# Kernel tuning notes

Measured on AMD Instinct MI355X. Metric: run time of the kernel, lower is better.

Reference implementation:

```python
import jax, jax.numpy as jnp
import numpy as np

B, SQ, SK, TT, DM, H, HKV, D, FF = 1, 2048, 3072, 4096, 2048, 16, 8, 128, 6144
EPS = 1e-6
THETA = 1000000.0

def rmsnorm(x, w):
    v = jnp.mean(x * x, axis=-1, keepdims=True)
    return x * jax.lax.rsqrt(v + EPS) * w

def rope_cos_sin(pos):
    inv = 1.0 / (THETA ** (jnp.arange(0, D, 2, dtype=jnp.float32) / D))
    f = pos.astype(jnp.float32)[..., None] * inv  # [B,S,D/2]
    emb = jnp.concatenate([f, f], axis=-1)        # [B,S,D]
    return jnp.cos(emb), jnp.sin(emb)

def rotate_half(x):
    x1, x2 = jnp.split(x, 2, axis=-1)
    return jnp.concatenate([-x2, x1], axis=-1)

def apply_rope(x, cos, sin):  # x: [B,H,S,D]; cos/sin: [B,S,D]
    return x * cos[:, None] + rotate_half(x) * sin[:, None]

def setup_inputs() -> dict:
    ks = jax.random.split(jax.random.key(0), 16)
    p = lambda i, sh: jax.random.normal(ks[i], sh, jnp.float32) * 0.02
    sri = lambda i, sh, mx: jnp.sort(jax.random.randint(ks[i], sh, 0, mx))
    return dict(
        hidden_states=jax.random.normal(ks[0], (B, SQ, DM), jnp.float32),
        kv_hidden=jax.random.normal(ks[1], (B, SK, DM), jnp.float32),
        causal_mask=jax.random.normal(ks[2], (B, 1, TT, TT), jnp.float32),
        w_q=p(3, (DM, H * D)), w_k=p(4, (DM, HKV * D)), w_v=p(5, (DM, HKV * D)),
        w_o=p(6, (H * D, DM)),
        q_norm_w=jnp.ones((D,), jnp.float32), k_norm_w=jnp.ones((D,), jnp.float32),
        ln1_w=jnp.ones((DM,), jnp.float32), ln2_w=jnp.ones((DM,), jnp.float32),
        w_gate=p(7, (DM, FF)), w_up=p(8, (DM, FF)), w_down=p(9, (FF, DM)),
        positions=sri(10, (B, SQ), TT), kv_positions=sri(11, (B, SK), TT),
        hs_idxs=sri(12, (SQ,), TT), key_idxs=sri(13, (SK,), TT))

def reference(hidden_states, kv_hidden, causal_mask, w_q, w_k, w_v, w_o,
              q_norm_w, k_norm_w, ln1_w, ln2_w, w_gate, w_up, w_down,
              positions, kv_positions, hs_idxs, key_idxs):
    # irregular mask reconstruction: gather kv dim then query dim (dims 3 then 2)
    mask = causal_mask[:, :, :, key_idxs][:, :, hs_idxs, :]  # [B,1,SQ,SK]
    # input_layernorm (RMSNorm)
    h = rmsnorm(hidden_states, ln1_w)
    hk = rmsnorm(kv_hidden, ln1_w)
    # Qwen3 attention: proj + per-head RMSNorm on q/k + RoPE + GQA
    q = rmsnorm((h @ w_q).reshape(B, SQ, H, D), q_norm_w).transpose(0, 2, 1, 3)
    k = rmsnorm((hk @ w_k).reshape(B, SK, HKV, D), k_norm_w).transpose(0, 2, 1, 3)
    v = (hk @ w_v).reshape(B, SK, HKV, D).transpose(0, 2, 1, 3)
    cq, sq = rope_cos_sin(positions)
    ck, sk = rope_cos_sin(kv_positions)
    q = apply_rope(q, cq, sq)
    k = apply_rope(k, ck, sk)
    rep = H // HKV
    k = jnp.repeat(k, rep, axis=1)
    v = jnp.repeat(v, rep, axis=1)
    scores = jnp.einsum('bhqd,bhkd->bhqk', q, k) * (D ** -0.5) + mask
    attn = jax.nn.softmax(scores, axis=-1)
    ctx = jnp.einsum('bhqk,bhkd->bhqd', attn, v).transpose(0, 2, 1, 3).reshape(B, SQ, H * D)
    hidden = hidden_states + ctx @ w_o
    # post-attention RMSNorm + SwiGLU MLP
    h2 = rmsnorm(hidden, ln2_w)
    mlp = (jax.nn.silu(h2 @ w_gate) * (h2 @ w_up)) @ w_down
    return hidden + mlp
```

## Files before the change

### kernel.cpp

```cpp
#include <hip/hip_runtime.h>
#include <math.h>

constexpr int SQ = 2048, SK = 3072, TT = 4096, DM = 2048;
constexpr int H = 16, HKV = 8, D = 128, FF = 6144;
#define EPS 1e-6f

typedef __attribute__((ext_vector_type(8))) short short8;
typedef __attribute__((ext_vector_type(4))) float f32x4;

#define GLOBAL_AS __attribute__((address_space(1)))
#define LDS_AS __attribute__((address_space(3)))

__device__ __forceinline__ unsigned short f2bf(float f) {
  unsigned u = __float_as_uint(f);
  unsigned r = (u + 0x7fffu + ((u >> 16) & 1u)) >> 16;
  return (unsigned short)r;
}
__device__ __forceinline__ float bflo(unsigned w) { return __uint_as_float(w << 16); }
__device__ __forceinline__ float bfhi(unsigned w) { return __uint_as_float(w & 0xffff0000u); }

__global__ __launch_bounds__(256) void wt_bf16_kernel(
    const float* __restrict__ w, unsigned short* __restrict__ wT, int K, int N) {
  __shared__ unsigned short s[64][73];
  int n0 = blockIdx.x * 64, k0 = blockIdx.y * 64;
  int tid = threadIdx.x;
  int cn = (tid & 15) * 4, rk = tid >> 4;
#pragma unroll
  for (int p = 0; p < 4; p++) {
    int k = rk + p * 16;
    const float4 f = *(const float4*)&w[(size_t)(k0 + k) * N + n0 + cn];
    s[k][cn] = f2bf(f.x); s[k][cn + 1] = f2bf(f.y);
    s[k][cn + 2] = f2bf(f.z); s[k][cn + 3] = f2bf(f.w);
  }
  __syncthreads();
  int ck = (tid & 15) * 4, rn = tid >> 4;
#pragma unroll
  for (int p = 0; p < 4; p++) {
    int n = rn + p * 16;
    ushort4 o;
    o.x = s[ck][n]; o.y = s[ck + 1][n]; o.z = s[ck + 2][n]; o.w = s[ck + 3][n];
    *(ushort4*)&wT[(size_t)(n0 + n) * K + k0 + ck] = o;
  }
}

__global__ __launch_bounds__(256) void vtrans_kernel(
    const float* __restrict__ vb, unsigned short* __restrict__ vt) {
  __shared__ unsigned short s[64][72];
  int kv0 = blockIdx.x * 64, d0 = blockIdx.y * 64, kvh = blockIdx.z;
  int tid = threadIdx.x;
  int cd = (tid & 15) * 4, rk = tid >> 4;
#pragma unroll
  for (int p = 0; p < 4; p++) {
    int kv = rk + p * 16;
    const float4 f = *(const float4*)&vb[((size_t)(kv0 + kv) * HKV + kvh) * D + d0 + cd];
    s[kv][cd] = f2bf(f.x); s[kv][cd + 1] = f2bf(f.y);
    s[kv][cd + 2] = f2bf(f.z); s[kv][cd + 3] = f2bf(f.w);
  }
  __syncthreads();
  int ck = (tid & 15) * 4, rd = tid >> 4;
#pragma unroll
  for (int p = 0; p < 4; p++) {
    int d = rd + p * 16;
    ushort4 o;
    o.x = s[ck][d]; o.y = s[ck + 1][d]; o.z = s[ck + 2][d]; o.w = s[ck + 3][d];
    *(ushort4*)&vt[((size_t)kvh * D + d0 + d) * SK + kv0 + ck] = o;
  }
}

__global__ __launch_bounds__(256) void rmsnorm_bf16_kernel(
    const float* __restrict__ x, const float* __restrict__ w,
    unsigned short* __restrict__ y) {
  int row = blockIdx.x;
  const float* xr = x + (size_t)row * DM;
  int c = threadIdx.x * 8;
  float4 a = *(const float4*)&xr[c];
  float4 b = *(const float4*)&xr[c + 4];
  float ss = a.x * a.x + a.y * a.y + a.z * a.z + a.w * a.w +
             b.x * b.x + b.y * b.y + b.z * b.z + b.w * b.w;
  for (int o = 32; o > 0; o >>= 1) ss += __shfl_down(ss, o);
  __shared__ float sred[4];
  int lane = threadIdx.x & 63, wid = threadIdx.x >> 6;
  if (lane == 0) sred[wid] = ss;
  __syncthreads();
  if (threadIdx.x == 0)
    sred[0] = rsqrtf((sred[0] + sred[1] + sred[2] + sred[3]) * (1.0f / (float)DM) + EPS);
  __syncthreads();
  float sc = sred[0];
  float4 wa = *(const float4*)&w[c];
  float4 wb = *(const float4*)&w[c + 4];
  ushort4 o1, o2;
  o1.x = f2bf(a.x * sc * wa.x); o1.y = f2bf(a.y * sc * wa.y);
  o1.z = f2bf(a.z * sc * wa.z); o1.w = f2bf(a.w * sc * wa.w);
  o2.x = f2bf(b.x * sc * wb.x); o2.y = f2bf(b.y * sc * wb.y);
  o2.z = f2bf(b.z * sc * wb.z); o2.w = f2bf(b.w * sc * wb.w);
  unsigned short* yr = y + (size_t)row * DM + c;
  *(ushort4*)&yr[0] = o1;
  *(ushort4*)&yr[4] = o2;
}

template <bool ADD, bool OUTBF>
__global__ __launch_bounds__(256) void mgemm_kernel(
    const unsigned short* __restrict__ A, const unsigned short* __restrict__ BT,
    const float* __restrict__ Add, void* __restrict__ Cp,
    int M, int N, int K) {
  __shared__ unsigned short As[128 * 64];
  __shared__ unsigned short Bs[128 * 64];
  const int tid = threadIdx.x;
  const int wave = tid >> 6, lane = tid & 63;
  const int bm = blockIdx.y * 128, bn = blockIdx.x * 128;
  const int wr = wave >> 1, wc = wave & 1;
  const int fl = lane & 15, fk = lane >> 4;

  const int srow = wave * 8 + (lane >> 3);
  const int schunk = (lane & 7) ^ (srow & 7);
  const unsigned short* Abase = A + (size_t)(bm + srow) * K + schunk * 8;
  const unsigned short* Bbase = BT + (size_t)(bn + srow) * K + schunk * 8;

  f32x4 acc[4][4];
#pragma unroll
  for (int m = 0; m < 4; m++)
#pragma unroll
    for (int n = 0; n < 4; n++)
#pragma unroll
      for (int e = 0; e < 4; e++) acc[m][n][e] = 0.f;

  for (int k0 = 0; k0 < K; k0 += 64) {
#pragma unroll
    for (int p = 0; p < 4; p++) {
      __builtin_amdgcn_global_load_lds(
          (GLOBAL_AS unsigned*)(Abase + (size_t)(p * 32) * K + k0),
          (LDS_AS unsigned*)&As[(p * 32 + wave * 8) * 64], 16, 0, 0);
      __builtin_amdgcn_global_load_lds(
          (GLOBAL_AS unsigned*)(Bbase + (size_t)(p * 32) * K + k0),
          (LDS_AS unsigned*)&Bs[(p * 32 + wave * 8) * 64], 16, 0, 0);
    }
    __syncthreads();
#pragma unroll
    for (int kk = 0; kk < 2; kk++) {
      short8 a_[4], b_[4];
#pragma unroll
      for (int m = 0; m < 4; m++) {
        int row = wr * 64 + m * 16 + fl;
        int ch = (kk * 4 + fk) ^ (row & 7);
        a_[m] = *(const short8*)&As[row * 64 + ch * 8];
      }
#pragma unroll
      for (int n = 0; n < 4; n++) {
        int row = wc * 64 + n * 16 + fl;
        int ch = (kk * 4 + fk) ^ (row & 7);
        b_[n] = *(const short8*)&Bs[row * 64 + ch * 8];
      }
#pragma unroll
      for (int m = 0; m < 4; m++)
#pragma unroll
        for (int n = 0; n < 4; n++)
          acc[m][n] = __builtin_amdgcn_mfma_f32_16x16x32_bf16(
              a_[m], b_[n], acc[m][n], 0, 0, 0);
    }
    __syncthreads();
  }

#pragma unroll
  for (int m = 0; m < 4; m++) {
    int row0 = bm + wr * 64 + m * 16 + fk * 4;
#pragma unroll
    for (int n = 0; n < 4; n++) {
      int col = bn + wc * 64 + n * 16 + fl;
#pragma unroll
      for (int r = 0; r < 4; r++) {
        size_t idx = (size_t)(row0 + r) * N + col;
        float v = acc[m][n][r];
        if (ADD) v += Add[idx];
        if (OUTBF) ((unsigned short*)Cp)[idx] = f2bf(v);
        else ((float*)Cp)[idx] = v;
      }
    }
  }
}

__global__ __launch_bounds__(128) void qknorm_rope_bf16_kernel(
    const float* __restrict__ x, const float* __restrict__ nw,
    const int* __restrict__ pos, unsigned short* __restrict__ out,
    int nheads, int S) {
  int s = blockIdx.x, hh = blockIdx.y;
  const float* xr = x + ((size_t)s * nheads + hh) * D;
  int d = threadIdx.x;
  float vv = xr[d];
  float ss = vv * vv;
  for (int o = 32; o > 0; o >>= 1) ss += __shfl_down(ss, o);
  __shared__ float sred[2];
  __shared__ float sn[D];
  if ((d & 63) == 0) sred[d >> 6] = ss;
  __syncthreads();
  float ms = (sred[0] + sred[1]) * (1.0f / (float)D);
  float n = vv * rsqrtf(ms + EPS) * nw[d];
  sn[d] = n;
  __syncthreads();
  int t = d & 63;
  float inv = powf(1000000.0f, -((float)(2 * t)) / (float)D);
  float ang = (float)pos[s] * inv;
  float c = cosf(ang), si = sinf(ang);
  float rh = (d < 64) ? -sn[d + 64] : sn[d - 64];
  out[((size_t)hh * S + s) * D + d] = f2bf(n * c + rh * si);
}

__global__ __launch_bounds__(256) void mask_gather_kernel(
    const float* __restrict__ mask, const int* __restrict__ hs_idxs,
    const int* __restrict__ key_idxs, float* __restrict__ maskg) {
  int q = blockIdx.x;
  const float* base = mask + (size_t)hs_idxs[q] * TT;
  float* out = maskg + (size_t)q * SK;
  for (int j = threadIdx.x; j < SK; j += 256) out[j] = base[key_idxs[j]];
}

__global__ __launch_bounds__(256) void attn_mfma_kernel(
    const unsigned short* __restrict__ qbf, const unsigned short* __restrict__ kbf,
    const unsigned short* __restrict__ vtbf, const float* __restrict__ maskg,
    unsigned short* __restrict__ ctx) {
  __shared__ unsigned short Ks[2][64 * 128];
  __shared__ unsigned short Vts[2][128 * 64];
  __shared__ unsigned short Pl[4][16 * 72];

  const int tid = threadIdx.x;
  const int wave = tid >> 6, lane = tid & 63;
  const int fl = lane & 15, g = lane >> 4;
  const float scale = 0.08838834764831845f;

  int bid = blockIdx.x;
  int swz = (bid & 7) * 64 + (bid >> 3);
  const int hh = swz >> 5;
  const int qblk = (swz & 31) * 64;
  const int kvh = hh >> 1;

  short8 qf[4];
  {
    const unsigned short* qrow = qbf + ((size_t)hh * SQ + qblk + wave * 16 + fl) * D;
#pragma unroll
    for (int kw = 0; kw < 4; kw++) qf[kw] = *(const short8*)&qrow[kw * 32 + g * 8];
  }

  const unsigned short* ksrc[4];
  const unsigned short* vsrc[4];
  {
    int krow = lane >> 4;
    int vrow = lane >> 3;
    int vcs = (lane & 7) ^ vrow;
#pragma unroll
    for (int p = 0; p < 4; p++) {
      int rowk = wave * 16 + p * 4 + krow;
      int kcs = (lane & 15) ^ (rowk & 7);
      ksrc[p] = kbf + ((size_t)kvh * SK + rowk) * D + kcs * 8;
      int rowv = wave * 32 + p * 8 + vrow;
      vsrc[p] = vtbf + ((size_t)kvh * D + rowv) * SK + vcs * 8;
    }
  }
  const float* mbase = maskg + (size_t)(qblk + wave * 16 + fl) * SK + g * 4;

  float m_i = -INFINITY, l_i = 0.f;
  f32x4 o[8];
#pragma unroll
  for (int n = 0; n < 8; n++)
#pragma unroll
    for (int r = 0; r < 4; r++) o[n][r] = 0.f;

#define STAGE(bufi)                                                            \
  {                                                                            \
    _Pragma("unroll")                                                          \
    for (int p = 0; p < 4; p++) {                                              \
      __builtin_amdgcn_global_load_lds(                                        \
          (GLOBAL_AS unsigned*)ksrc[p],                                        \
          (LDS_AS unsigned*)&Ks[bufi][(wave * 16 + p * 4) * 128], 16, 0, 0);   \
      __builtin_amdgcn_global_load_lds(                                        \
          (GLOBAL_AS unsigned*)vsrc[p],                                        \
          (LDS_AS unsigned*)&Vts[bufi][(wave * 32 + p * 8) * 64], 16, 0, 0);   \
      ksrc[p] += 64 * D;                                                       \
      vsrc[p] += 64;                                                           \
    }                                                                          \
  }

  STAGE(0);
  __syncthreads();

  const int NT = SK / 64;
  for (int t = 0; t < NT; t++) {
    const int buf = t & 1;
    if (t + 1 < NT) STAGE(buf ^ 1);

    float4 mv[4];
#pragma unroll
    for (int kvf = 0; kvf < 4; kvf++) mv[kvf] = *(const float4*)(mbase + kvf * 16);
    mbase += 64;

    f32x4 sa[4];
#pragma unroll
    for (int kvf = 0; kvf < 4; kvf++)
#pragma unroll
      for (int r = 0; r < 4; r++) sa[kvf][r] = 0.f;
#pragma unroll
    for (int kw = 0; kw < 4; kw++) {
#pragma unroll
      for (int kvf = 0; kvf < 4; kvf++) {
        int row = kvf * 16 + fl;
        int ch = (kw * 4 + g) ^ (fl & 7);
        short8 kf = *(const short8*)&Ks[buf][row * 128 + ch * 8];
        sa[kvf] = __builtin_amdgcn_mfma_f32_16x16x32_bf16(kf, qf[kw], sa[kvf], 0, 0, 0);
      }
    }

    float p4[4][4];
    float rm = -INFINITY;
#pragma unroll
    for (int kvf = 0; kvf < 4; kvf++) {
      p4[kvf][0] = sa[kvf][0] * scale + mv[kvf].x;
      p4[kvf][1] = sa[kvf][1] * scale + mv[kvf].y;
      p4[kvf][2] = sa[kvf][2] * scale + mv[kvf].z;
      p4[kvf][3] = sa[kvf][3] * scale + mv[kvf].w;
#pragma unroll
      for (int r = 0; r < 4; r++) rm = fmaxf(rm, p4[kvf][r]);
    }
    rm = fmaxf(rm, __shfl_xor(rm, 16));
    rm = fmaxf(rm, __shfl_xor(rm, 32));
    float mn = fmaxf(m_i, rm);
    float alpha = __expf(m_i - mn);
    m_i = mn;
    float rs = 0.f;
#pragma unroll
    for (int kvf = 0; kvf < 4; kvf++) {
#pragma unroll
      for (int r = 0; r < 4; r++) { p4[kvf][r] = __expf(p4[kvf][r] - mn); rs += p4[kvf][r]; }
      ushort4 pk;
      pk.x = f2bf(p4[kvf][0]); pk.y = f2bf(p4[kvf][1]);
      pk.z = f2bf(p4[kvf][2]); pk.w = f2bf(p4[kvf][3]);
      *(ushort4*)&Pl[wave][fl * 72 + kvf * 16 + g * 4] = pk;
    }
    rs += __shfl_xor(rs, 16);
    rs += __shfl_xor(rs, 32);
    l_i = l_i * alpha + rs;

    float av[4];
#pragma unroll
    for (int r = 0; r < 4; r++) av[r] = __shfl(alpha, 4 * g + r);
#pragma unroll
    for (int n = 0; n < 8; n++)
#pragma unroll
      for (int r = 0; r < 4; r++) o[n][r] *= av[r];

#pragma unroll
    for (int k = 0; k < 2; k++) {
      short8 pf = *(const short8*)&Pl[wave][fl * 72 + k * 32 + g * 8];
#pragma unroll
      for (int n = 0; n < 8; n++) {
        int row = n * 16 + fl;
        int ch = (k * 4 + g) ^ (fl & 7);
        short8 vf = *(const short8*)&Vts[buf][row * 64 + ch * 8];
        o[n] = __builtin_amdgcn_mfma_f32_16x16x32_bf16(pf, vf, o[n], 0, 0, 0);
      }
    }
    __syncthreads();
  }

#pragma unroll
  for (int r = 0; r < 4; r++) {
    float linv = 1.f / __shfl(l_i, 4 * g + r);
    size_t base = ((size_t)(qblk + wave * 16 + 4 * g + r)) * (H * D) + (size_t)hh * D + fl;
#pragma unroll
    for (int n = 0; n < 8; n++) ctx[base + n * 16] = f2bf(o[n][r] * linv);
  }
#undef STAGE
}

__device__ __forceinline__ unsigned silu2(unsigned gw, unsigned uw) {
  float g0 = bflo(gw), g1 = bfhi(gw), u0 = bflo(uw), u1 = bfhi(uw);
  float r0 = g0 / (1.f + __expf(-g0)) * u0;
  float r1 = g1 / (1.f + __expf(-g1)) * u1;
  return ((unsigned)f2bf(r1) << 16) | f2bf(r0);
}
__global__ __launch_bounds__(256) void silu_mul_bf16_kernel(
    unsigned short* __restrict__ g, const unsigned short* __restrict__ u, int n8) {
  int i = blockIdx.x * 256 + threadIdx.x;
  if (i >= n8) return;
  uint4 G = *(const uint4*)&g[(size_t)i * 8];
  uint4 U = *(const uint4*)&u[(size_t)i * 8];
  G.x = silu2(G.x, U.x); G.y = silu2(G.y, U.y);
  G.z = silu2(G.z, U.z); G.w = silu2(G.w, U.w);
  *(uint4*)&g[(size_t)i * 8] = G;
}

extern "C" void kernel_launch(void* const* d_in, const int* in_sizes, int n_in,
                              void* d_out, int out_size, void* d_ws, size_t ws_size,
                              hipStream_t stream) {
  (void)in_sizes; (void)n_in; (void)out_size; (void)ws_size;
  const float* hidden_states = (const float*)d_in[0];
  const float* kv_hidden     = (const float*)d_in[1];
  const float* causal_mask   = (const float*)d_in[2];
  const float* w_q      = (const float*)d_in[3];
  const float* w_k      = (const float*)d_in[4];
  const float* w_v      = (const float*)d_in[5];
  const float* w_o      = (const float*)d_in[6];
  const float* q_norm_w = (const float*)d_in[7];
  const float* k_norm_w = (const float*)d_in[8];
  const float* ln1_w    = (const float*)d_in[9];
  const float* ln2_w    = (const float*)d_in[10];
  const float* w_gate   = (const float*)d_in[11];
  const float* w_up     = (const float*)d_in[12];
  const float* w_down   = (const float*)d_in[13];
  const int* positions    = (const int*)d_in[14];
  const int* kv_positions = (const int*)d_in[15];
  const int* hs_idxs      = (const int*)d_in[16];
  const int* key_idxs     = (const int*)d_in[17];

  char* wsb = (char*)d_ws;
  float* maskg           = (float*)(wsb + 0);
  unsigned short* h_bf   = (unsigned short*)(wsb + 25165824);
  unsigned short* hk_bf  = (unsigned short*)(wsb + 33554432);
  unsigned short* W1     = (unsigned short*)(wsb + 46137344);
  unsigned short* W2     = (unsigned short*)(wsb + 71303168);
  float* qb              = (float*)(wsb + 96468992);
  float* kb              = (float*)(wsb + 113246208);
  float* vb              = (float*)(wsb + 125829120);
  unsigned short* ctx_bf = (unsigned short*)(wsb + 138412032);
  unsigned short* gate_bf = (unsigned short*)wsb;
  unsigned short* up_bf   = (unsigned short*)(wsb + 113246208);
  float* hidden           = qb;
  unsigned short* h2_bf   = h_bf;
  unsigned short* qbf    = (unsigned short*)(wsb + 46137344);
  unsigned short* kbf    = (unsigned short*)(wsb + 54525952);
  unsigned short* vtbf   = (unsigned short*)(wsb + 60817408);

  mask_gather_kernel<<<SQ, 256, 0, stream>>>(causal_mask, hs_idxs, key_idxs, maskg);
  rmsnorm_bf16_kernel<<<SQ, 256, 0, stream>>>(hidden_states, ln1_w, h_bf);
  rmsnorm_bf16_kernel<<<SK, 256, 0, stream>>>(kv_hidden, ln1_w, hk_bf);

  wt_bf16_kernel<<<dim3((H * D) / 64, DM / 64), 256, 0, stream>>>(w_q, W1, DM, H * D);
  wt_bf16_kernel<<<dim3((HKV * D) / 64, DM / 64), 256, 0, stream>>>(w_k, W2, DM, HKV * D);
  mgemm_kernel<false, false><<<dim3((H * D) / 128, SQ / 128), 256, 0, stream>>>(
      h_bf, W1, nullptr, qb, SQ, H * D, DM);
  mgemm_kernel<false, false><<<dim3((HKV * D) / 128, SK / 128), 256, 0, stream>>>(
      hk_bf, W2, nullptr, kb, SK, HKV * D, DM);
  wt_bf16_kernel<<<dim3((HKV * D) / 64, DM / 64), 256, 0, stream>>>(w_v, W1, DM, HKV * D);
  mgemm_kernel<false, false><<<dim3((HKV * D) / 128, SK / 128), 256, 0, stream>>>(
      hk_bf, W1, nullptr, vb, SK, HKV * D, DM);

  qknorm_rope_bf16_kernel<<<dim3(SQ, H), 128, 0, stream>>>(
      qb, q_norm_w, positions, qbf, H, SQ);
  qknorm_rope_bf16_kernel<<<dim3(SK, HKV), 128, 0, stream>>>(
      kb, k_norm_w, kv_positions, kbf, HKV, SK);
  vtrans_kernel<<<dim3(SK / 64, D / 64, HKV), 256, 0, stream>>>(vb, vtbf);

  attn_mfma_kernel<<<512, 256, 0, stream>>>(qbf, kbf, vtbf, maskg, ctx_bf);

  wt_bf16_kernel<<<dim3(DM / 64, (H * D) / 64), 256, 0, stream>>>(w_o, W2, H * D, DM);
  mgemm_kernel<true, false><<<dim3(DM / 128, SQ / 128), 256, 0, stream>>>(
      ctx_bf, W2, hidden_states, hidden, SQ, DM, H * D);

  rmsnorm_bf16_kernel<<<SQ, 256, 0, stream>>>(hidden, ln2_w, h2_bf);
  wt_bf16_kernel<<<dim3(FF / 64, DM / 64), 256, 0, stream>>>(w_gate, W1, DM, FF);
  wt_bf16_kernel<<<dim3(FF / 64, DM / 64), 256, 0, stream>>>(w_up, W2, DM, FF);
  mgemm_kernel<false, true><<<dim3(FF / 128, SQ / 128), 256, 0, stream>>>(
      h2_bf, W1, nullptr, gate_bf, SQ, FF, DM);
  mgemm_kernel<false, true><<<dim3(FF / 128, SQ / 128), 256, 0, stream>>>(
      h2_bf, W2, nullptr, up_bf, SQ, FF, DM);
  silu_mul_bf16_kernel<<<(SQ * FF / 8 + 255) / 256, 256, 0, stream>>>(
      gate_bf, up_bf, SQ * FF / 8);

  wt_bf16_kernel<<<dim3(DM / 64, FF / 64), 256, 0, stream>>>(w_down, W1, FF, DM);
  mgemm_kernel<true, false><<<dim3(DM / 128, SQ / 128), 256, 0, stream>>>(
      gate_bf, W1, hidden, (float*)d_out, SQ, DM, FF);
}
```

Measured before the change: 892.1 us.

## Split-K small GEMMs with atomics, fuse K/V and gate/up GEMMs, lazy softmax rescale

The Q, O and down projections now use a split-K GEMM that accumulates into pre-zeroed or pre-copied fp32 outputs with atomic adds. This fills more compute units, since these grids had only 256 tiles. K and V projections are merged into one GEMM over concatenated weights, and gate and up are computed in a single launch with a dual-output GEMM. The attention kernel skips the running-max rescale unless some row's max grows by more than 8, which avoids extra exps and multiplies at the cost of reduced numerical headroom. The atomics make accumulation order nondeterministic, and the new zero and copy passes add memory traffic.

```diff
diff --git a/kernel.cpp b/kernel.cpp
--- a/kernel.cpp
+++ b/kernel.cpp
@@ -44,7 +44,7 @@
 }
 
 __global__ __launch_bounds__(256) void vtrans_kernel(
-    const float* __restrict__ vb, unsigned short* __restrict__ vt) {
+    const float* __restrict__ vb, int ldv, unsigned short* __restrict__ vt) {
   __shared__ unsigned short s[64][72];
   int kv0 = blockIdx.x * 64, d0 = blockIdx.y * 64, kvh = blockIdx.z;
   int tid = threadIdx.x;
@@ -52,7 +52,7 @@
 #pragma unroll
   for (int p = 0; p < 4; p++) {
     int kv = rk + p * 16;
-    const float4 f = *(const float4*)&vb[((size_t)(kv0 + kv) * HKV + kvh) * D + d0 + cd];
+    const float4 f = *(const float4*)&vb[(size_t)(kv0 + kv) * ldv + kvh * D + d0 + cd];
     s[kv][cd] = f2bf(f.x); s[kv][cd + 1] = f2bf(f.y);
     s[kv][cd + 2] = f2bf(f.z); s[kv][cd + 3] = f2bf(f.w);
   }
@@ -98,23 +98,29 @@
   *(ushort4*)&yr[4] = o2;
 }
 
-template <bool ADD, bool OUTBF>
+template <bool OUTBF>
 __global__ __launch_bounds__(256) void mgemm_kernel(
-    const unsigned short* __restrict__ A, const unsigned short* __restrict__ BT,
-    const float* __restrict__ Add, void* __restrict__ Cp,
+    const unsigned short* __restrict__ A, const unsigned short* __restrict__ BT1,
+    const unsigned short* __restrict__ BT2, int N1,
+    void* __restrict__ C1p, void* __restrict__ C2p, int ld1, int ld2,
     int M, int N, int K) {
   __shared__ unsigned short As[128 * 64];
   __shared__ unsigned short Bs[128 * 64];
   const int tid = threadIdx.x;
   const int wave = tid >> 6, lane = tid & 63;
   const int bm = blockIdx.y * 128, bn = blockIdx.x * 128;
+  const bool second = bn >= N1;
+  const unsigned short* BT = second ? BT2 : BT1;
+  const int bnl = second ? bn - N1 : bn;
+  void* Cp = second ? C2p : C1p;
+  const int ldc = second ? ld2 : ld1;
   const int wr = wave >> 1, wc = wave & 1;
   const int fl = lane & 15, fk = lane >> 4;
 
   const int srow = wave * 8 + (lane >> 3);
   const int schunk = (lane & 7) ^ (srow & 7);
   const unsigned short* Abase = A + (size_t)(bm + srow) * K + schunk * 8;
-  const unsigned short* Bbase = BT + (size_t)(bn + srow) * K + schunk * 8;
+  const unsigned short* Bbase = BT + (size_t)(bnl + srow) * K + schunk * 8;
 
   f32x4 acc[4][4];
 #pragma unroll
@@ -165,12 +171,11 @@
     int row0 = bm + wr * 64 + m * 16 + fk * 4;
 #pragma unroll
     for (int n = 0; n < 4; n++) {
-      int col = bn + wc * 64 + n * 16 + fl;
+      int col = bnl + wc * 64 + n * 16 + fl;
 #pragma unroll
       for (int r = 0; r < 4; r++) {
-        size_t idx = (size_t)(row0 + r) * N + col;
+        size_t idx = (size_t)(row0 + r) * ldc + col;
         float v = acc[m][n][r];
-        if (ADD) v += Add[idx];
         if (OUTBF) ((unsigned short*)Cp)[idx] = f2bf(v);
         else ((float*)Cp)[idx] = v;
       }
@@ -178,12 +183,95 @@
   }
 }
 
+__global__ __launch_bounds__(256) void msplit_kernel(
+    const unsigned short* __restrict__ A, const unsigned short* __restrict__ BT,
+    float* __restrict__ C, int M, int N, int K, int kchunk) {
+  __shared__ unsigned short As[128 * 64];
+  __shared__ unsigned short Bs[128 * 64];
+  const int tid = threadIdx.x;
+  const int wave = tid >> 6, lane = tid & 63;
+  const int bm = blockIdx.y * 128, bn = blockIdx.x * 128;
+  const int kbeg = blockIdx.z * kchunk, kend = kbeg + kchunk;
+  const int wr = wave >> 1, wc = wave & 1;
+  const int fl = lane & 15, fk = lane >> 4;
+
+  const int srow = wave * 8 + (lane >> 3);
+  const int schunk = (lane & 7) ^ (srow & 7);
+  const unsigned short* Abase = A + (size_t)(bm + srow) * K + schunk * 8;
+  const unsigned short* Bbase = BT + (size_t)(bn + srow) * K + schunk * 8;
+
+  f32x4 acc[4][4];
+#pragma unroll
+  for (int m = 0; m < 4; m++)
+#pragma unroll
+    for (int n = 0; n < 4; n++)
+#pragma unroll
+      for (int e = 0; e < 4; e++) acc[m][n][e] = 0.f;
+
+  for (int k0 = kbeg; k0 < kend; k0 += 64) {
+#pragma unroll
+    for (int p = 0; p < 4; p++) {
+      __builtin_amdgcn_global_load_lds(
+          (GLOBAL_AS unsigned*)(Abase + (size_t)(p * 32) * K + k0),
+          (LDS_AS unsigned*)&As[(p * 32 + wave * 8) * 64], 16, 0, 0);
+      __builtin_amdgcn_global_load_lds(
+          (GLOBAL_AS unsigned*)(Bbase + (size_t)(p * 32) * K + k0),
+          (LDS_AS unsigned*)&Bs[(p * 32 + wave * 8) * 64], 16, 0, 0);
+    }
+    __syncthreads();
+#pragma unroll
+    for (int kk = 0; kk < 2; kk++) {
+      short8 a_[4], b_[4];
+#pragma unroll
+      for (int m = 0; m < 4; m++) {
+        int row = wr * 64 + m * 16 + fl;
+        int ch = (kk * 4 + fk) ^ (row & 7);
+        a_[m] = *(const short8*)&As[row * 64 + ch * 8];
+      }
+#pragma unroll
+      for (int n = 0; n < 4; n++) {
+        int row = wc * 64 + n * 16 + fl;
+        int ch = (kk * 4 + fk) ^ (row & 7);
+        b_[n] = *(const short8*)&Bs[row * 64 + ch * 8];
+      }
+#pragma unroll
+      for (int m = 0; m < 4; m++)
+#pragma unroll
+        for (int n = 0; n < 4; n++)
+          acc[m][n] = __builtin_amdgcn_mfma_f32_16x16x32_bf16(
+              a_[m], b_[n], acc[m][n], 0, 0, 0);
+    }
+    __syncthreads();
+  }
+
+#pragma unroll
+  for (int m = 0; m < 4; m++) {
+    int row0 = bm + wr * 64 + m * 16 + fk * 4;
+#pragma unroll
+    for (int n = 0; n < 4; n++) {
+      int col = bn + wc * 64 + n * 16 + fl;
+#pragma unroll
+      for (int r = 0; r < 4; r++)
+        unsafeAtomicAdd(&C[(size_t)(row0 + r) * N + col], acc[m][n][r]);
+    }
+  }
+}
+
+__global__ __launch_bounds__(256) void zero4_kernel(float4* __restrict__ p, int n4) {
+  int i = blockIdx.x * 256 + threadIdx.x;
+  if (i < n4) p[i] = make_float4(0.f, 0.f, 0.f, 0.f);
+}
+__global__ __launch_bounds__(256) void copy4_kernel(
+    float4* __restrict__ d, const float4* __restrict__ s, int n4) {
+  int i = blockIdx.x * 256 + threadIdx.x;
+  if (i < n4) d[i] = s[i];
+}
+
 __global__ __launch_bounds__(128) void qknorm_rope_bf16_kernel(
-    const float* __restrict__ x, const float* __restrict__ nw,
-    const int* __restrict__ pos, unsigned short* __restrict__ out,
-    int nheads, int S) {
+    const float* __restrict__ x, int ldx, const float* __restrict__ nw,
+    const int* __restrict__ pos, unsigned short* __restrict__ out, int S) {
   int s = blockIdx.x, hh = blockIdx.y;
-  const float* xr = x + ((size_t)s * nheads + hh) * D;
+  const float* xr = x + (size_t)s * ldx + hh * D;
   int d = threadIdx.x;
   float vv = xr[d];
   float ss = vv * vv;
@@ -320,8 +408,9 @@
     }
     rm = fmaxf(rm, __shfl_xor(rm, 16));
     rm = fmaxf(rm, __shfl_xor(rm, 32));
-    float mn = fmaxf(m_i, rm);
-    float alpha = __expf(m_i - mn);
+    const int need = __any(rm > m_i + 8.f);
+    float mn = need ? fmaxf(m_i, rm) : m_i;
+    float alpha = need ? __expf(m_i - mn) : 1.f;
     m_i = mn;
     float rs = 0.f;
 #pragma unroll
@@ -337,13 +426,15 @@
     rs += __shfl_xor(rs, 32);
     l_i = l_i * alpha + rs;
 
-    float av[4];
-#pragma unroll
-    for (int r = 0; r < 4; r++) av[r] = __shfl(alpha, 4 * g + r);
-#pragma unroll
-    for (int n = 0; n < 8; n++)
-#pragma unroll
-      for (int r = 0; r < 4; r++) o[n][r] *= av[r];
+    if (need) {
+      float av[4];
+#pragma unroll
+      for (int r = 0; r < 4; r++) av[r] = __shfl(alpha, 4 * g + r);
+#pragma unroll
+      for (int n = 0; n < 8; n++)
+#pragma unroll
+        for (int r = 0; r < 4; r++) o[n][r] *= av[r];
+    }
 
 #pragma unroll
     for (int k = 0; k < 2; k++) {
@@ -413,57 +504,64 @@
   float* maskg           = (float*)(wsb + 0);
   unsigned short* h_bf   = (unsigned short*)(wsb + 25165824);
   unsigned short* hk_bf  = (unsigned short*)(wsb + 33554432);
-  unsigned short* W1     = (unsigned short*)(wsb + 46137344);
-  unsigned short* W2     = (unsigned short*)(wsb + 71303168);
-  float* qb              = (float*)(wsb + 96468992);
-  float* kb              = (float*)(wsb + 113246208);
-  float* vb              = (float*)(wsb + 125829120);
-  unsigned short* ctx_bf = (unsigned short*)(wsb + 138412032);
-  unsigned short* gate_bf = (unsigned short*)wsb;
-  unsigned short* up_bf   = (unsigned short*)(wsb + 113246208);
-  float* hidden           = qb;
-  unsigned short* h2_bf   = h_bf;
-  unsigned short* qbf    = (unsigned short*)(wsb + 46137344);
-  unsigned short* kbf    = (unsigned short*)(wsb + 54525952);
-  unsigned short* vtbf   = (unsigned short*)(wsb + 60817408);
+  unsigned short* Wq     = (unsigned short*)(wsb + 46137344);
+  unsigned short* Wkv    = (unsigned short*)(wsb + 54525952);
+  float* qb              = (float*)(wsb + 62914560);
+  float* kvb             = (float*)(wsb + 79691776);
+  unsigned short* qbf    = (unsigned short*)(wsb + 104857600);
+  unsigned short* kbf    = (unsigned short*)(wsb + 113246208);
+  unsigned short* vtbf   = (unsigned short*)(wsb + 119537664);
+  unsigned short* ctx_bf = (unsigned short*)(wsb + 125829120);
+  float* hidden          = qb;
+  unsigned short* Wo     = Wq;
+  unsigned short* h2_bf  = h_bf;
+  unsigned short* Wg     = (unsigned short*)(wsb + 0);
+  unsigned short* Wu     = (unsigned short*)(wsb + 79691776);
+  unsigned short* gate_bf = (unsigned short*)(wsb + 104857600);
+  unsigned short* up_bf  = (unsigned short*)(wsb + 33554432);
+  unsigned short* Wd     = (unsigned short*)(wsb + 33554432);
 
   mask_gather_kernel<<<SQ, 256, 0, stream>>>(causal_mask, hs_idxs, key_idxs, maskg);
   rmsnorm_bf16_kernel<<<SQ, 256, 0, stream>>>(hidden_states, ln1_w, h_bf);
   rmsnorm_bf16_kernel<<<SK, 256, 0, stream>>>(kv_hidden, ln1_w, hk_bf);
 
-  wt_bf16_kernel<<<dim3((H * D) / 64, DM / 64), 256, 0, stream>>>(w_q, W1, DM, H * D);
-  wt_bf16_kernel<<<dim3((HKV * D) / 64, DM / 64), 256, 0, stream>>>(w_k, W2, DM, HKV * D);
-  mgemm_kernel<false, false><<<dim3((H * D) / 128, SQ / 128), 256, 0, stream>>>(
-      h_bf, W1, nullptr, qb, SQ, H * D, DM);
-  mgemm_kernel<false, false><<<dim3((HKV * D) / 128, SK / 128), 256, 0, stream>>>(
-      hk_bf, W2, nullptr, kb, SK, HKV * D, DM);
-  wt_bf16_kernel<<<dim3((HKV * D) / 64, DM / 64), 256, 0, stream>>>(w_v, W1, DM, HKV * D);
-  mgemm_kernel<false, false><<<dim3((HKV * D) / 128, SK / 128), 256, 0, stream>>>(
-      hk_bf, W1, nullptr, vb, SK, HKV * D, DM);
+  wt_bf16_kernel<<<dim3((H * D) / 64, DM / 64), 256, 0, stream>>>(w_q, Wq, DM, H * D);
+  wt_bf16_kernel<<<dim3((HKV * D) / 64, DM / 64), 256, 0, stream>>>(w_k, Wkv, DM, HKV * D);
+  wt_bf16_kernel<<<dim3((HKV * D) / 64, DM / 64), 256, 0, stream>>>(
+      w_v, Wkv + (size_t)(HKV * D) * DM, DM, HKV * D);
+
+  zero4_kernel<<<(SQ * H * D / 4 + 255) / 256, 256, 0, stream>>>((float4*)qb, SQ * H * D / 4);
+  msplit_kernel<<<dim3((H * D) / 128, SQ / 128, 2), 256, 0, stream>>>(
+      h_bf, Wq, qb, SQ, H * D, DM, DM / 2);
+  mgemm_kernel<false><<<dim3((2 * HKV * D) / 128, SK / 128), 256, 0, stream>>>(
+      hk_bf, Wkv, nullptr, 2 * HKV * D, kvb, nullptr, 2 * HKV * D, 0, SK, 2 * HKV * D, DM);
 
   qknorm_rope_bf16_kernel<<<dim3(SQ, H), 128, 0, stream>>>(
-      qb, q_norm_w, positions, qbf, H, SQ);
+      qb, H * D, q_norm_w, positions, qbf, SQ);
   qknorm_rope_bf16_kernel<<<dim3(SK, HKV), 128, 0, stream>>>(
-      kb, k_norm_w, kv_positions, kbf, HKV, SK);
-  vtrans_kernel<<<dim3(SK / 64, D / 64, HKV), 256, 0, stream>>>(vb, vtbf);
+      kvb, 2 * HKV * D, k_norm_w, kv_positions, kbf, SK);
+  vtrans_kernel<<<dim3(SK / 64, D / 64, HKV), 256, 0, stream>>>(
+      kvb + HKV * D, 2 * HKV * D, vtbf);
 
   attn_mfma_kernel<<<512, 256, 0, stream>>>(qbf, kbf, vtbf, maskg, ctx_bf);
 
-  wt_bf16_kernel<<<dim3(DM / 64, (H * D) / 64), 256, 0, stream>>>(w_o, W2, H * D, DM);
-  mgemm_kernel<true, false><<<dim3(DM / 128, SQ / 128), 256, 0, stream>>>(
-      ctx_bf, W2, hidden_states, hidden, SQ, DM, H * D);
+  copy4_kernel<<<(SQ * DM / 4 + 255) / 256, 256, 0, stream>>>(
+      (float4*)hidden, (const float4*)hidden_states, SQ * DM / 4);
+  wt_bf16_kernel<<<dim3(DM / 64, (H * D) / 64), 256, 0, stream>>>(w_o, Wo, H * D, DM);
+  msplit_kernel<<<dim3(DM / 128, SQ / 128, 2), 256, 0, stream>>>(
+      ctx_bf, Wo, hidden, SQ, DM, H * D, (H * D) / 2);
 
   rmsnorm_bf16_kernel<<<SQ, 256, 0, stream>>>(hidden, ln2_w, h2_bf);
-  wt_bf16_kernel<<<dim3(FF / 64, DM / 64), 256, 0, stream>>>(w_gate, W1, DM, FF);
-  wt_bf16_kernel<<<dim3(FF / 64, DM / 64), 256, 0, stream>>>(w_up, W2, DM, FF);
-  mgemm_kernel<false, true><<<dim3(FF / 128, SQ / 128), 256, 0, stream>>>(
-      h2_bf, W1, nullptr, gate_bf, SQ, FF, DM);
-  mgemm_kernel<false, true><<<dim3(FF / 128, SQ / 128), 256, 0, stream>>>(
-      h2_bf, W2, nullptr, up_bf, SQ, FF, DM);
+  wt_bf16_kernel<<<dim3(FF / 64, DM / 64), 256, 0, stream>>>(w_gate, Wg, DM, FF);
+  wt_bf16_kernel<<<dim3(FF / 64, DM / 64), 256, 0, stream>>>(w_up, Wu, DM, FF);
+  mgemm_kernel<true><<<dim3((2 * FF) / 128, SQ / 128), 256, 0, stream>>>(
+      h2_bf, Wg, Wu, FF, gate_bf, up_bf, FF, FF, SQ, 2 * FF, DM);
   silu_mul_bf16_kernel<<<(SQ * FF / 8 + 255) / 256, 256, 0, stream>>>(
       gate_bf, up_bf, SQ * FF / 8);
 
-  wt_bf16_kernel<<<dim3(DM / 64, FF / 64), 256, 0, stream>>>(w_down, W1, FF, DM);
-  mgemm_kernel<true, false><<<dim3(DM / 128, SQ / 128), 256, 0, stream>>>(
-      gate_bf, W1, hidden, (float*)d_out, SQ, DM, FF);
-}
+  wt_bf16_kernel<<<dim3(DM / 64, FF / 64), 256, 0, stream>>>(w_down, Wd, FF, DM);
+  copy4_kernel<<<(SQ * DM / 4 + 255) / 256, 256, 0, stream>>>(
+      (float4*)d_out, (const float4*)hidden, SQ * DM / 4);
+  msplit_kernel<<<dim3(DM / 128, SQ / 128, 3), 256, 0, stream>>>(
+      gate_bf, Wd, (float*)d_out, SQ, DM, FF, FF / 3);
+}
```

New measurement: 873.7 us. 2.1% less time.
